# Optimization experiments

Hardware: AMD Instinct MI355X
Metric: run time of the kernel (lower is better)

## Reference

```python
import jax, jax.numpy as jnp
import numpy as np

EMBD = 256
HEAD = 4
HD = EMBD // HEAD  # 64
EPS = 1e-5


def setup_inputs() -> dict:
    key = jax.random.key(0)
    ks = jax.random.split(key, 12)
    s = lambda fan_in: 1.0 / np.sqrt(fan_in)
    return {
        "x": jax.random.normal(ks[0], (16, 1024, EMBD), dtype=jnp.float32),
        # attention params (stored as [in, out])
        "qkv_w": jax.random.uniform(ks[1], (EMBD, 3 * EMBD), jnp.float32, -s(EMBD), s(EMBD)),
        "qkv_b": jax.random.uniform(ks[2], (3 * EMBD,), jnp.float32, -s(EMBD), s(EMBD)),
        "out_w": jax.random.uniform(ks[3], (EMBD, EMBD), jnp.float32, -s(EMBD), s(EMBD)),
        "out_b": jax.random.uniform(ks[4], (EMBD,), jnp.float32, -s(EMBD), s(EMBD)),
        # MLP params
        "fc_w": jax.random.uniform(ks[5], (EMBD, 4 * EMBD), jnp.float32, -s(EMBD), s(EMBD)),
        "fc_b": jax.random.uniform(ks[6], (4 * EMBD,), jnp.float32, -s(EMBD), s(EMBD)),
        "proj_w": jax.random.uniform(ks[7], (4 * EMBD, EMBD), jnp.float32, -s(4 * EMBD), s(4 * EMBD)),
        "proj_b": jax.random.uniform(ks[8], (EMBD,), jnp.float32, -s(4 * EMBD), s(4 * EMBD)),
        # LayerNorm params
        "ln1_g": jnp.ones((EMBD,), jnp.float32),
        "ln1_b": jnp.zeros((EMBD,), jnp.float32),
        "ln2_g": jnp.ones((EMBD,), jnp.float32),
        "ln2_b": jnp.zeros((EMBD,), jnp.float32),
    }


def layer_norm(x, g, b):
    mu = jnp.mean(x, axis=-1, keepdims=True)
    var = jnp.mean(jnp.square(x - mu), axis=-1, keepdims=True)
    return (x - mu) * jax.lax.rsqrt(var + EPS) * g + b


def block_forward(x, qkv_w, qkv_b, out_w, out_b, fc_w, fc_b, proj_w, proj_b,
                  ln1_g, ln1_b, ln2_g, ln2_b):
    B, S, E = x.shape
    # --- attention branch ---
    h = layer_norm(x, ln1_g, ln1_b)
    qkv = h @ qkv_w + qkv_b                       # [B,S,3E]
    q, k, v = jnp.split(qkv, 3, axis=-1)
    q = q.reshape(B, S, HEAD, HD).transpose(0, 2, 1, 3)  # [B,H,S,D]
    k = k.reshape(B, S, HEAD, HD).transpose(0, 2, 1, 3)
    v = v.reshape(B, S, HEAD, HD).transpose(0, 2, 1, 3)
    att = jnp.einsum('bhqd,bhkd->bhqk', q, k) / jnp.sqrt(jnp.float32(HD))
    causal = jnp.tril(jnp.ones((S, S), dtype=bool))
    att = jnp.where(causal, att, -jnp.inf)
    att = jax.nn.softmax(att, axis=-1)
    o = jnp.einsum('bhqk,bhkd->bhqd', att, v)     # [B,H,S,D]
    o = o.transpose(0, 2, 1, 3).reshape(B, S, E)
    x = x + o @ out_w + out_b
    # --- MLP branch (dropout inactive at eval) ---
    h = layer_norm(x, ln2_g, ln2_b)
    h = jax.nn.relu(h @ fc_w + fc_b)
    x = x + h @ proj_w + proj_b
    return x


def reference(x, qkv_w, qkv_b, out_w, out_b, fc_w, fc_b, proj_w, proj_b,
              ln1_g, ln1_b, ln2_g, ln2_b):
    return block_forward(x, qkv_w, qkv_b, out_w, out_b, fc_w, fc_b,
                         proj_w, proj_b, ln1_g, ln1_b, ln2_g, ln2_b)
```

## Files before the change

kernel.cpp:

```cpp
#include <hip/hip_runtime.h>
#include <cstdint>


using f32x4  = __attribute__((ext_vector_type(4))) float;
using f32x16 = __attribute__((ext_vector_type(16))) float;
using s16x8  = __attribute__((ext_vector_type(8))) short;
using s16x4  = __attribute__((ext_vector_type(4))) short;

__device__ inline short f2bf(float f) {
    union { float f; unsigned u; } v{f};
    unsigned r = (v.u + 0x7FFFu + ((v.u >> 16) & 1u)) >> 16;
    return (short)r;
}

__device__ inline int cvt_pk_bf16(float lo, float hi) {
    int d;
    asm("v_cvt_pk_bf16_f32 %0, %1, %2" : "=v"(d) : "v"(lo), "v"(hi));
    return d;
}
__device__ inline void swap32(int& a, int& b) {
    asm("v_permlane32_swap_b32 %0, %1" : "+v"(a), "+v"(b));
}

__device__ inline void gload16(const void* g, void* l) {
    __builtin_amdgcn_global_load_lds(
        (const __attribute__((address_space(1))) void*)g,
        (__attribute__((address_space(3))) void*)l, 16, 0, 0);
}

__global__ __launch_bounds__(256) void prep_kernel(
    const float* __restrict__ qkv_w, const float* __restrict__ out_w,
    const float* __restrict__ fc_w,  const float* __restrict__ proj_w,
    short* __restrict__ wt_qkv, short* __restrict__ wt_out,
    short* __restrict__ wt_fc,  short* __restrict__ wt_proj,
    const float* __restrict__ x, const float* __restrict__ ln1_g,
    const float* __restrict__ ln1_b, short* __restrict__ hout)
{
    __shared__ short T[64][65];
    int id  = blockIdx.x;
    int tid = threadIdx.x;

    if (id < 192) {
        const float* W; short* Wt; int K, N, nt, kt;
        if (id < 48)       { W = qkv_w;  Wt = wt_qkv;  K = 256;  N = 768;  nt = id % 12;        kt = id / 12; }
        else if (id < 64)  { W = out_w;  Wt = wt_out;  K = 256;  N = 256;  nt = (id - 48) & 3;  kt = (id - 48) >> 2; }
        else if (id < 128) { W = fc_w;   Wt = wt_fc;   K = 256;  N = 1024; nt = (id - 64) & 15; kt = (id - 64) >> 4; }
        else               { W = proj_w; Wt = wt_proj; K = 1024; N = 256;  nt = (id - 128) & 3; kt = (id - 128) >> 2; }
        int n0 = nt * 64, k0 = kt * 64;
        int r = tid >> 2, c = (tid & 3) << 4;
        const float* src = W + (size_t)(k0 + r) * N + n0 + c;
#pragma unroll
        for (int u = 0; u < 4; ++u) {
            float4 v = *reinterpret_cast<const float4*>(src + u * 4);
            T[r][c + u * 4 + 0] = f2bf(v.x);
            T[r][c + u * 4 + 1] = f2bf(v.y);
            T[r][c + u * 4 + 2] = f2bf(v.z);
            T[r][c + u * 4 + 3] = f2bf(v.w);
        }
        __syncthreads();
        s16x8 o0, o1;
#pragma unroll
        for (int jj = 0; jj < 8; ++jj) { o0[jj] = T[c + jj][r]; o1[jj] = T[c + 8 + jj][r]; }
        short* dst = Wt + (size_t)(n0 + r) * K + k0 + c;
        *reinterpret_cast<s16x8*>(dst)     = o0;
        *reinterpret_cast<s16x8*>(dst + 8) = o1;
    } else {
        int lane = tid & 63;
        int row  = (id - 192) * 4 + (tid >> 6);
        const float* xr = x + (size_t)row * 256;
        float4 v = *reinterpret_cast<const float4*>(xr + lane * 4);
        float s = v.x + v.y + v.z + v.w;
#pragma unroll
        for (int o2 = 32; o2 >= 1; o2 >>= 1) s += __shfl_xor(s, o2);
        float mu = s * (1.0f / 256.0f);
        float dx = v.x - mu, dy = v.y - mu, dz = v.z - mu, dw = v.w - mu;
        float q = dx * dx + dy * dy + dz * dz + dw * dw;
#pragma unroll
        for (int o2 = 32; o2 >= 1; o2 >>= 1) q += __shfl_xor(q, o2);
        float rstd = rsqrtf(q * (1.0f / 256.0f) + 1e-5f);
        float4 gv = *reinterpret_cast<const float4*>(ln1_g + lane * 4);
        float4 bv = *reinterpret_cast<const float4*>(ln1_b + lane * 4);
        s16x4 ov;
        ov[0] = f2bf(dx * rstd * gv.x + bv.x);
        ov[1] = f2bf(dy * rstd * gv.y + bv.y);
        ov[2] = f2bf(dz * rstd * gv.z + bv.z);
        ov[3] = f2bf(dw * rstd * gv.w + bv.w);
        *reinterpret_cast<s16x4*>(hout + (size_t)row * 256 + lane * 4) = ov;
    }
}

template <int RELU, int RES, int OBF16, int BM, int QKV, int DBUF>
__global__ __launch_bounds__(256) void mgemm_kernel(const short* __restrict__ A,
                                                    const short* __restrict__ Bt,
                                                    const float* __restrict__ bias,
                                                    const float* __restrict__ R,
                                                    void* __restrict__ Cv,
                                                    short* __restrict__ vt,
                                                    int N, int K)
{
    constexpr int MI  = BM / 32;
    constexpr int ASZ = BM * 64;
    constexpr int BSZ = 128 * 64;
    __shared__ short As[(1 + DBUF) * ASZ];
    __shared__ short Bs[(1 + DBUF) * BSZ];

    int tid = threadIdx.x;
    int l   = tid & 63;
    int w   = tid >> 6;
    int lr  = l & 15;
    int lk8 = (l >> 4) << 3;
    int r4  = (l >> 4) << 2;
    int wr  = w >> 1, wc = w & 1;
    int bn  = blockIdx.x * 128, bm = blockIdx.y * BM;

    int scolS = ((l & 7) << 3) ^ ((l >> 3) << 3);
    int srowA = w * (BM / 4) + (l >> 3);
    int srowB = (w << 5) + (l >> 3);
    const short* pa = A  + (size_t)(bm + srowA) * K + scolS;
    const short* pb = Bt + (size_t)(bn + srowB) * K + scolS;
    short* dstA = As + w * (BM / 4) * 64;
    short* dstB = Bs + (w << 11);

    f32x4 acc[MI][4];
#pragma unroll
    for (int mi = 0; mi < MI; ++mi)
#pragma unroll
        for (int ni = 0; ni < 4; ++ni) acc[mi][ni] = (f32x4){0.f, 0.f, 0.f, 0.f};

    int swz = (lr & 7) << 3;
    int cur = 0;

    if (DBUF) {
#pragma unroll
        for (int i = 0; i < BM / 32; ++i)
            gload16(pa + (size_t)(i * 8) * K, dstA + (i << 9));
#pragma unroll
        for (int i = 0; i < 4; ++i)
            gload16(pb + (size_t)(i * 8) * K, dstB + (i << 9));
        __syncthreads();
    }

    for (int k0 = 0; k0 < K; k0 += 64) {
        if (DBUF) {
            if (k0 + 64 < K) {
                int nxt = cur ^ 1;
#pragma unroll
                for (int i = 0; i < BM / 32; ++i)
                    gload16(pa + (size_t)(i * 8) * K + k0 + 64, dstA + nxt * ASZ + (i << 9));
#pragma unroll
                for (int i = 0; i < 4; ++i)
                    gload16(pb + (size_t)(i * 8) * K + k0 + 64, dstB + nxt * BSZ + (i << 9));
            }
        } else {
            __syncthreads();
#pragma unroll
            for (int i = 0; i < BM / 32; ++i)
                gload16(pa + (size_t)(i * 8) * K + k0, dstA + (i << 9));
#pragma unroll
            for (int i = 0; i < 4; ++i)
                gload16(pb + (size_t)(i * 8) * K + k0, dstB + (i << 9));
            __syncthreads();
        }
        const short* curA = As + cur * ASZ;
        const short* curB = Bs + cur * BSZ;
#pragma unroll
        for (int ks = 0; ks < 2; ++ks) {
            s16x8 af[MI], bf[4];
#pragma unroll
            for (int mi = 0; mi < MI; ++mi) {
                int row = wr * (BM / 2) + (mi << 4) + lr;
                af[mi] = *reinterpret_cast<const s16x8*>(
                    &curA[(row << 6) + (((ks << 5) + lk8) ^ swz)]);
            }
#pragma unroll
            for (int ni = 0; ni < 4; ++ni) {
                int row = (wc << 6) + (ni << 4) + lr;
                bf[ni] = *reinterpret_cast<const s16x8*>(
                    &curB[(row << 6) + (((ks << 5) + lk8) ^ swz)]);
            }
            __builtin_amdgcn_s_setprio(1);
#pragma unroll
            for (int mi = 0; mi < MI; ++mi)
#pragma unroll
                for (int ni = 0; ni < 4; ++ni)
                    acc[mi][ni] = __builtin_amdgcn_mfma_f32_16x16x32_bf16(
                        af[mi], bf[ni], acc[mi][ni], 0, 0, 0);
            __builtin_amdgcn_s_setprio(0);
        }
        if (DBUF) {
            __syncthreads();
            cur ^= 1;
        }
    }

    float bv[4];
#pragma unroll
    for (int ni = 0; ni < 4; ++ni)
        bv[ni] = bias[bn + (wc << 6) + (ni << 4) + lr];

#pragma unroll
    for (int mi = 0; mi < MI; ++mi) {
#pragma unroll
        for (int ni = 0; ni < 4; ++ni) {
            int n = bn + (wc << 6) + (ni << 4) + lr;
#pragma unroll
            for (int r = 0; r < 4; ++r) {
                int m = bm + wr * (BM / 2) + (mi << 4) + r4 + r;
                float v = acc[mi][ni][r] + bv[ni];
                if (RELU) v = fmaxf(v, 0.0f);
                if (RES)  v += R[(size_t)m * N + n];
                if (QKV) {
                    if (bn < 512) {
                        ((short*)Cv)[(size_t)m * 512 + n] = f2bf(v);
                    } else {
                        int hh = (n - 512) >> 6, dd = (n - 512) & 63;
                        int bb = m >> 10, ss = m & 1023;
                        vt[(size_t)((((bb << 2) | hh) << 6) | dd) * 1024 + ss] = f2bf(v);
                    }
                } else if (OBF16) {
                    ((short*)Cv)[(size_t)m * N + n] = f2bf(v);
                } else {
                    ((float*)Cv)[(size_t)m * N + n] = v;
                }
            }
        }
    }
}

__global__ __launch_bounds__(256) void oproj_ln_kernel(const short* __restrict__ A,
                                                       const short* __restrict__ Bt,
                                                       const float* __restrict__ bias,
                                                       const float* __restrict__ R,
                                                       float* __restrict__ x1,
                                                       short* __restrict__ h2,
                                                       const float* __restrict__ g,
                                                       const float* __restrict__ bb)
{
    constexpr int ASZ = 64 * 64;
    constexpr int BSZ = 256 * 64;
    __shared__ short As[2 * ASZ];
    __shared__ short Bs[2 * BSZ];

    int tid = threadIdx.x;
    int l   = tid & 63;
    int w   = tid >> 6;
    int lr  = l & 15;
    int lk8 = (l >> 4) << 3;
    int r4  = (l >> 4) << 2;
    int bm  = blockIdx.x * 64;

    int scolS = ((l & 7) << 3) ^ ((l >> 3) << 3);
    const short* pa = A  + (size_t)(bm + (w << 4) + (l >> 3)) * 256 + scolS;
    const short* pb = Bt + (size_t)((w << 6) + (l >> 3)) * 256 + scolS;
    short* dstA = As + (w << 10);
    short* dstB = Bs + (w << 12);

    f32x4 acc[16];
#pragma unroll
    for (int ni = 0; ni < 16; ++ni) acc[ni] = (f32x4){0.f, 0.f, 0.f, 0.f};

    int swz = (lr & 7) << 3;

#pragma unroll
    for (int i = 0; i < 2; ++i)
        gload16(pa + (size_t)(i * 8) * 256, dstA + (i << 9));
#pragma unroll
    for (int i = 0; i < 8; ++i)
        gload16(pb + (size_t)(i * 8) * 256, dstB + (i << 9));
    __syncthreads();

    int cur = 0;
    for (int k0 = 0; k0 < 256; k0 += 64) {
        if (k0 + 64 < 256) {
            int nxt = cur ^ 1;
#pragma unroll
            for (int i = 0; i < 2; ++i)
                gload16(pa + (size_t)(i * 8) * 256 + k0 + 64, dstA + nxt * ASZ + (i << 9));
#pragma unroll
            for (int i = 0; i < 8; ++i)
                gload16(pb + (size_t)(i * 8) * 256 + k0 + 64, dstB + nxt * BSZ + (i << 9));
        }
        const short* curA = As + cur * ASZ;
        const short* curB = Bs + cur * BSZ;
#pragma unroll
        for (int ks = 0; ks < 2; ++ks) {
            int arow = (w << 4) + lr;
            s16x8 af = *reinterpret_cast<const s16x8*>(
                &curA[(arow << 6) + (((ks << 5) + lk8) ^ swz)]);
            __builtin_amdgcn_s_setprio(1);
#pragma unroll
            for (int ni = 0; ni < 16; ++ni) {
                int row = (ni << 4) + lr;
                s16x8 bf = *reinterpret_cast<const s16x8*>(
                    &curB[(row << 6) + (((ks << 5) + lk8) ^ swz)]);
                acc[ni] = __builtin_amdgcn_mfma_f32_16x16x32_bf16(af, bf, acc[ni], 0, 0, 0);
            }
            __builtin_amdgcn_s_setprio(0);
        }
        __syncthreads();
        cur ^= 1;
    }

#pragma unroll
    for (int ni = 0; ni < 16; ++ni) {
        int n = (ni << 4) + lr;
        float bvx = bias[n];
#pragma unroll
        for (int r = 0; r < 4; ++r) {
            int m = bm + (w << 4) + r4 + r;
            acc[ni][r] += bvx + R[(size_t)m * 256 + n];
        }
    }
#pragma unroll
    for (int r = 0; r < 4; ++r) {
        float s = 0.0f;
#pragma unroll
        for (int ni = 0; ni < 16; ++ni) s += acc[ni][r];
        s += __shfl_xor(s, 1); s += __shfl_xor(s, 2);
        s += __shfl_xor(s, 4); s += __shfl_xor(s, 8);
        float mu = s * (1.0f / 256.0f);
        float q = 0.0f;
#pragma unroll
        for (int ni = 0; ni < 16; ++ni) {
            float d = acc[ni][r] - mu;
            q += d * d;
        }
        q += __shfl_xor(q, 1); q += __shfl_xor(q, 2);
        q += __shfl_xor(q, 4); q += __shfl_xor(q, 8);
        float rstd = rsqrtf(q * (1.0f / 256.0f) + 1e-5f);

        int m = bm + (w << 4) + r4 + r;
#pragma unroll
        for (int ni = 0; ni < 16; ++ni) {
            int n = (ni << 4) + lr;
            float v = acc[ni][r];
            x1[(size_t)m * 256 + n] = v;
            h2[(size_t)m * 256 + n] = f2bf((v - mu) * rstd * g[n] + bb[n]);
        }
    }
}

__global__ __launch_bounds__(256, 2) void attn_kernel(const short* __restrict__ qk,
                                                      const short* __restrict__ vt,
                                                      short* __restrict__ o)
{
    constexpr int KSZ = 128 * 64;
    constexpr int VSZ = 64 * 128;
    __shared__ short Ks[2 * KSZ];
    __shared__ short Vs[2 * VSZ];

    int bid  = blockIdx.x;
    int xcd  = bid & 7;
    int j    = bid >> 3;
    int bhg  = j & 7;
    int qidx = j >> 3;
    int qt   = qidx < 4 ? qidx : 11 - qidx;
    int bh   = (bhg << 3) | xcd;
    int b = bh >> 2, h = bh & 3;

    int tid = threadIdx.x;
    int l   = tid & 63;
    int w   = tid >> 6;
    int lq  = l & 31;
    int hg  = l >> 5;

    int krow0 = (w << 3) + (l >> 3);
    int kscol = ((l & 7) << 3) ^ (((l >> 3) & 7) << 3);
    const short* kgp = qk + (size_t)(b * 1024 + krow0) * 512 + 256 + h * 64 + kscol;
    short* dstK = Ks + (w << 3) * 64;
    int vrow0 = (w << 2) + (l >> 4);
    int vscol = ((l & 15) << 3) ^ ((vrow0 & 7) << 3);
    const short* vgp = vt + (size_t)((bh << 6) + vrow0) * 1024 + vscol;
    short* dstV = Vs + (w << 2) * 128;

    const float SC = 0.125f * 1.44269504088896f;

    const short* qrow = qk + (size_t)(b * 1024 + qt * 128 + (w << 5) + lq) * 512
                        + h * 64 + (hg << 3);
    s16x8 qf[4];
#pragma unroll
    for (int ds = 0; ds < 4; ++ds)
        qf[ds] = *reinterpret_cast<const s16x8*>(qrow + 16 * ds);

#pragma unroll
    for (int i = 0; i < 4; ++i) {
        gload16(kgp + (size_t)(i * 32) * 512, dstK + i * 32 * 64);
        gload16(vgp + (size_t)(i * 16) * 1024, dstV + i * 16 * 128);
    }
    __syncthreads();

    float m = -1e30f, lsum = 0.0f;
    f32x16 oacc[2];
#pragma unroll
    for (int dt = 0; dt < 2; ++dt)
#pragma unroll
        for (int r = 0; r < 16; ++r) oacc[dt][r] = 0.0f;
    int qglob = qt * 128 + (w << 5) + lq;
    int cur = 0;
    int niter = qt + 1;

    for (int kt = 0; kt < niter; ++kt) {
        if (kt + 1 < niter) {
            int nxt = cur ^ 1;
#pragma unroll
            for (int i = 0; i < 4; ++i) {
                gload16(kgp + (size_t)((kt + 1) * 128 + i * 32) * 512,
                        dstK + nxt * KSZ + i * 32 * 64);
                gload16(vgp + (size_t)(i * 16) * 1024 + (kt + 1) * 128,
                        dstV + nxt * VSZ + i * 16 * 128);
            }
        }

        f32x16 sv[4];
#pragma unroll
        for (int jt = 0; jt < 4; ++jt)
#pragma unroll
            for (int r = 0; r < 16; ++r) sv[jt][r] = 0.0f;
        __builtin_amdgcn_s_setprio(1);
#pragma unroll
        for (int ds = 0; ds < 4; ++ds) {
#pragma unroll
            for (int jt = 0; jt < 4; ++jt) {
                int row = jt * 32 + lq;
                s16x8 kf = *reinterpret_cast<const s16x8*>(
                    &Ks[cur * KSZ + (row << 6) + ((16 * ds + (hg << 3)) ^ ((row & 7) << 3))]);
                sv[jt] = __builtin_amdgcn_mfma_f32_32x32x16_bf16(kf, qf[ds], sv[jt], 0, 0, 0);
            }
        }
        __builtin_amdgcn_s_setprio(0);
#pragma unroll
        for (int jt = 0; jt < 4; ++jt)
#pragma unroll
            for (int r = 0; r < 16; ++r) sv[jt][r] *= SC;

        if (kt == niter - 1) {
#pragma unroll
            for (int jt = 0; jt < 4; ++jt)
#pragma unroll
                for (int r = 0; r < 16; ++r) {
                    int kg = kt * 128 + jt * 32 + (r & 3) + ((r >> 2) << 3) + (hg << 2);
                    if (kg > qglob) sv[jt][r] = -1e30f;
                }
        }

        float rm = -1e30f;
#pragma unroll
        for (int jt = 0; jt < 4; ++jt)
#pragma unroll
            for (int r = 0; r < 16; ++r) rm = fmaxf(rm, sv[jt][r]);
        rm = fmaxf(rm, __shfl_xor(rm, 32));
        bool big = __any(rm > m + 8.0f);
        float fct = 1.0f;
        if (big) {
            float mn = fmaxf(m, rm);
            fct = exp2f(m - mn);
            m = mn;
        }
        float ps = 0.0f;
#pragma unroll
        for (int jt = 0; jt < 4; ++jt)
#pragma unroll
            for (int r = 0; r < 16; ++r) {
                float p = exp2f(sv[jt][r] - m);
                sv[jt][r] = p;
                ps += p;
            }
        ps += __shfl_xor(ps, 32);
        lsum = lsum * fct + ps;

        if (big) {
#pragma unroll
            for (int r = 0; r < 16; ++r) {
                float f = __shfl(fct, (r & 3) + ((r >> 2) << 3) + (hg << 2));
                oacc[0][r] *= f;
                oacc[1][r] *= f;
            }
        }

#pragma unroll
        for (int jt = 0; jt < 4; ++jt) {
            int x0 = cvt_pk_bf16(sv[jt][0],  sv[jt][1]);
            int x1 = cvt_pk_bf16(sv[jt][2],  sv[jt][3]);
            int y0 = cvt_pk_bf16(sv[jt][4],  sv[jt][5]);
            int y1 = cvt_pk_bf16(sv[jt][6],  sv[jt][7]);
            int z0 = cvt_pk_bf16(sv[jt][8],  sv[jt][9]);
            int z1 = cvt_pk_bf16(sv[jt][10], sv[jt][11]);
            int w0 = cvt_pk_bf16(sv[jt][12], sv[jt][13]);
            int w1 = cvt_pk_bf16(sv[jt][14], sv[jt][15]);
            swap32(x0, y0); swap32(x1, y1);
            swap32(z0, w0); swap32(z1, w1);
            union { int i[4]; s16x8 v; } fA, fB;
            fA.i[0] = x0; fA.i[1] = x1; fA.i[2] = y0; fA.i[3] = y1;
            fB.i[0] = z0; fB.i[1] = z1; fB.i[2] = w0; fB.i[3] = w1;
            __builtin_amdgcn_s_setprio(1);
#pragma unroll
            for (int dt = 0; dt < 2; ++dt) {
                int row = dt * 32 + lq;
                int rs  = (row & 7) << 3;
                s16x8 vfA = *reinterpret_cast<const s16x8*>(
                    &Vs[cur * VSZ + (row << 7) + ((16 * (2 * jt)     + (hg << 3)) ^ rs)]);
                oacc[dt] = __builtin_amdgcn_mfma_f32_32x32x16_bf16(fA.v, vfA, oacc[dt], 0, 0, 0);
                s16x8 vfB = *reinterpret_cast<const s16x8*>(
                    &Vs[cur * VSZ + (row << 7) + ((16 * (2 * jt + 1) + (hg << 3)) ^ rs)]);
                oacc[dt] = __builtin_amdgcn_mfma_f32_32x32x16_bf16(fB.v, vfB, oacc[dt], 0, 0, 0);
            }
            __builtin_amdgcn_s_setprio(0);
        }

        if (kt + 1 < niter) {
            __syncthreads();
            cur ^= 1;
        }
    }

#pragma unroll
    for (int r = 0; r < 16; ++r) {
        int qr  = (r & 3) + ((r >> 2) << 3) + (hg << 2);
        float lv  = __shfl(lsum, qr);
        float inv = 1.0f / lv;
        int q = qt * 128 + (w << 5) + qr;
        short* orow = o + (size_t)(b * 1024 + q) * 256 + h * 64;
        orow[lq]      = f2bf(oacc[0][r] * inv);
        orow[32 + lq] = f2bf(oacc[1][r] * inv);
    }
}

extern "C" void kernel_launch(void* const* d_in, const int* in_sizes, int n_in,
                              void* d_out, int out_size, void* d_ws, size_t ws_size,
                              hipStream_t stream)
{
    const float* x      = (const float*)d_in[0];
    const float* qkv_w  = (const float*)d_in[1];
    const float* qkv_b  = (const float*)d_in[2];
    const float* out_w  = (const float*)d_in[3];
    const float* out_b  = (const float*)d_in[4];
    const float* fc_w   = (const float*)d_in[5];
    const float* fc_b   = (const float*)d_in[6];
    const float* proj_w = (const float*)d_in[7];
    const float* proj_b = (const float*)d_in[8];
    const float* ln1_g  = (const float*)d_in[9];
    const float* ln1_b  = (const float*)d_in[10];
    const float* ln2_g  = (const float*)d_in[11];
    const float* ln2_b  = (const float*)d_in[12];
    float* out = (float*)d_out;

    short* ws = (short*)d_ws;
    short* wt_qkv  = ws;
    short* wt_out  = ws + 196608;
    short* wt_fc   = ws + 262144;
    short* wt_proj = ws + 524288;
    short* bufA    = ws + 786432;
    short* qk_buf  = ws + 4980736;
    short* vt_buf  = ws + 13369344;
    short* h3_buf  = ws + 4980736;

    dim3 blk(256);

    prep_kernel<<<dim3(4288), blk, 0, stream>>>(
        qkv_w, out_w, fc_w, proj_w, wt_qkv, wt_out, wt_fc, wt_proj,
        x, ln1_g, ln1_b, bufA);
    mgemm_kernel<0, 0, 1, 128, 1, 0><<<dim3(6, 128), blk, 0, stream>>>(
        bufA, wt_qkv, qkv_b, nullptr, qk_buf, vt_buf, 768, 256);
    attn_kernel<<<dim3(512), blk, 0, stream>>>(qk_buf, vt_buf, bufA);
    oproj_ln_kernel<<<dim3(256), blk, 0, stream>>>(
        bufA, wt_out, out_b, x, out, bufA, ln2_g, ln2_b);
    mgemm_kernel<1, 0, 1, 128, 0, 0><<<dim3(8, 128), blk, 0, stream>>>(
        bufA, wt_fc, fc_b, nullptr, h3_buf, nullptr, 1024, 256);
    mgemm_kernel<0, 1, 0, 64, 0, 1><<<dim3(2, 256), blk, 0, stream>>>(
        h3_buf, wt_proj, proj_b, out, out, nullptr, 256, 1024);
}
```

Measured before the change: 119.3 us.

## Fuse MLP fc and proj GEMMs into one kernel keeping hidden activations on-chip

Replaces the separate fc+ReLU GEMM and the proj+residual GEMM with a single mlp_kernel. Each block owns 64 rows and loops over eight 128-wide chunks of the hidden dimension. The hidden tile is computed with MFMA, converted to bf16 and redistributed in registers through permlane swaps, then fed straight into the proj MFMAs. This removes the 16Kx1024 bf16 hidden-buffer round trip through global memory and one kernel launch. The cost is only 256 blocks, a large LDS footprint that limits occupancy, and weights re-streamed by every block with no double buffering. The generic GEMM is also specialized to the QKV path.

```diff
diff --git a/kernel.cpp b/kernel.cpp
--- a/kernel.cpp
+++ b/kernel.cpp
@@ -20,6 +20,9 @@
 }
 __device__ inline void swap32(int& a, int& b) {
     asm("v_permlane32_swap_b32 %0, %1" : "+v"(a), "+v"(b));
+}
+__device__ inline void swap16(int& a, int& b) {
+    asm("v_permlane16_swap_b32 %0, %1" : "+v"(a), "+v"(b));
 }
 
 __device__ inline void gload16(const void* g, void* l) {
@@ -89,20 +92,17 @@
     }
 }
 
-template <int RELU, int RES, int OBF16, int BM, int QKV, int DBUF>
-__global__ __launch_bounds__(256) void mgemm_kernel(const short* __restrict__ A,
-                                                    const short* __restrict__ Bt,
-                                                    const float* __restrict__ bias,
-                                                    const float* __restrict__ R,
-                                                    void* __restrict__ Cv,
-                                                    short* __restrict__ vt,
-                                                    int N, int K)
+template <int BM>
+__global__ __launch_bounds__(256) void qkv_gemm_kernel(const short* __restrict__ A,
+                                                       const short* __restrict__ Bt,
+                                                       const float* __restrict__ bias,
+                                                       short* __restrict__ qkout,
+                                                       short* __restrict__ vt,
+                                                       int N, int K)
 {
-    constexpr int MI  = BM / 32;
-    constexpr int ASZ = BM * 64;
-    constexpr int BSZ = 128 * 64;
-    __shared__ short As[(1 + DBUF) * ASZ];
-    __shared__ short Bs[(1 + DBUF) * BSZ];
+    constexpr int MI = BM / 32;
+    __shared__ short As[BM * 64];
+    __shared__ short Bs[128 * 64];
 
     int tid = threadIdx.x;
     int l   = tid & 63;
@@ -128,41 +128,17 @@
         for (int ni = 0; ni < 4; ++ni) acc[mi][ni] = (f32x4){0.f, 0.f, 0.f, 0.f};
 
     int swz = (lr & 7) << 3;
-    int cur = 0;
-
-    if (DBUF) {
+
+    for (int k0 = 0; k0 < K; k0 += 64) {
+        __syncthreads();
 #pragma unroll
         for (int i = 0; i < BM / 32; ++i)
-            gload16(pa + (size_t)(i * 8) * K, dstA + (i << 9));
+            gload16(pa + (size_t)(i * 8) * K + k0, dstA + (i << 9));
 #pragma unroll
         for (int i = 0; i < 4; ++i)
-            gload16(pb + (size_t)(i * 8) * K, dstB + (i << 9));
+            gload16(pb + (size_t)(i * 8) * K + k0, dstB + (i << 9));
         __syncthreads();
-    }
-
-    for (int k0 = 0; k0 < K; k0 += 64) {
-        if (DBUF) {
-            if (k0 + 64 < K) {
-                int nxt = cur ^ 1;
-#pragma unroll
-                for (int i = 0; i < BM / 32; ++i)
-                    gload16(pa + (size_t)(i * 8) * K + k0 + 64, dstA + nxt * ASZ + (i << 9));
-#pragma unroll
-                for (int i = 0; i < 4; ++i)
-                    gload16(pb + (size_t)(i * 8) * K + k0 + 64, dstB + nxt * BSZ + (i << 9));
-            }
-        } else {
-            __syncthreads();
-#pragma unroll
-            for (int i = 0; i < BM / 32; ++i)
-                gload16(pa + (size_t)(i * 8) * K + k0, dstA + (i << 9));
-#pragma unroll
-            for (int i = 0; i < 4; ++i)
-                gload16(pb + (size_t)(i * 8) * K + k0, dstB + (i << 9));
-            __syncthreads();
-        }
-        const short* curA = As + cur * ASZ;
-        const short* curB = Bs + cur * BSZ;
+
 #pragma unroll
         for (int ks = 0; ks < 2; ++ks) {
             s16x8 af[MI], bf[4];
@@ -170,13 +146,13 @@
             for (int mi = 0; mi < MI; ++mi) {
                 int row = wr * (BM / 2) + (mi << 4) + lr;
                 af[mi] = *reinterpret_cast<const s16x8*>(
-                    &curA[(row << 6) + (((ks << 5) + lk8) ^ swz)]);
+                    &As[(row << 6) + (((ks << 5) + lk8) ^ swz)]);
             }
 #pragma unroll
             for (int ni = 0; ni < 4; ++ni) {
                 int row = (wc << 6) + (ni << 4) + lr;
                 bf[ni] = *reinterpret_cast<const s16x8*>(
-                    &curB[(row << 6) + (((ks << 5) + lk8) ^ swz)]);
+                    &Bs[(row << 6) + (((ks << 5) + lk8) ^ swz)]);
             }
             __builtin_amdgcn_s_setprio(1);
 #pragma unroll
@@ -187,10 +163,6 @@
                         af[mi], bf[ni], acc[mi][ni], 0, 0, 0);
             __builtin_amdgcn_s_setprio(0);
         }
-        if (DBUF) {
-            __syncthreads();
-            cur ^= 1;
-        }
     }
 
     float bv[4];
@@ -207,20 +179,12 @@
             for (int r = 0; r < 4; ++r) {
                 int m = bm + wr * (BM / 2) + (mi << 4) + r4 + r;
                 float v = acc[mi][ni][r] + bv[ni];
-                if (RELU) v = fmaxf(v, 0.0f);
-                if (RES)  v += R[(size_t)m * N + n];
-                if (QKV) {
-                    if (bn < 512) {
-                        ((short*)Cv)[(size_t)m * 512 + n] = f2bf(v);
-                    } else {
-                        int hh = (n - 512) >> 6, dd = (n - 512) & 63;
-                        int bb = m >> 10, ss = m & 1023;
-                        vt[(size_t)((((bb << 2) | hh) << 6) | dd) * 1024 + ss] = f2bf(v);
-                    }
-                } else if (OBF16) {
-                    ((short*)Cv)[(size_t)m * N + n] = f2bf(v);
+                if (bn < 512) {
+                    qkout[(size_t)m * 512 + n] = f2bf(v);
                 } else {
-                    ((float*)Cv)[(size_t)m * N + n] = v;
+                    int hh = (n - 512) >> 6, dd = (n - 512) & 63;
+                    int bb = m >> 10, ss = m & 1023;
+                    vt[(size_t)((((bb << 2) | hh) << 6) | dd) * 1024 + ss] = f2bf(v);
                 }
             }
         }
@@ -340,6 +304,137 @@
     }
 }
 
+__global__ __launch_bounds__(256) void mlp_kernel(const short* __restrict__ h2,
+                                                  const short* __restrict__ wfc,
+                                                  const float* __restrict__ fcb,
+                                                  const short* __restrict__ w2,
+                                                  const float* __restrict__ pjb,
+                                                  const float* __restrict__ x1,
+                                                  float* __restrict__ out)
+{
+    __shared__ short H2s[4 * 64 * 64];
+    __shared__ short WFCs[128 * 64];
+    __shared__ short W2s[256 * 128];
+
+    int tid = threadIdx.x;
+    int l   = tid & 63;
+    int w   = tid >> 6;
+    int lr  = l & 15;
+    int lk8 = (l >> 4) << 3;
+    int r4  = (l >> 4) << 2;
+    int bm  = blockIdx.x * 64;
+    int swz = (lr & 7) << 3;
+
+    int scolS = ((l & 7) << 3) ^ ((l >> 3) << 3);
+
+    {
+        const short* pa = h2 + (size_t)(bm + (w << 4) + (l >> 3)) * 256 + scolS;
+#pragma unroll
+        for (int ks4 = 0; ks4 < 4; ++ks4)
+#pragma unroll
+            for (int i = 0; i < 2; ++i)
+                gload16(pa + (size_t)(i * 8) * 256 + ks4 * 64,
+                        H2s + ks4 * 4096 + (w << 10) + (i << 9));
+    }
+
+    int srowB = (w << 5) + (l >> 3);
+    const short* pwfc0 = wfc + (size_t)srowB * 256 + scolS;
+    short* dstWFC = WFCs + (w << 11);
+    int w2colS = ((l & 15) << 3) ^ ((((w << 2) + (l >> 4)) & 7) << 3);
+    const short* pw2 = w2 + (size_t)((w << 2) + (l >> 4)) * 1024 + w2colS;
+    short* dstW2 = W2s + (w << 9);
+
+    f32x4 acc[16];
+#pragma unroll
+    for (int ni = 0; ni < 16; ++ni) acc[ni] = (f32x4){0.f, 0.f, 0.f, 0.f};
+
+    for (int p = 0; p < 8; ++p) {
+        const short* pwfc = pwfc0 + (size_t)(p * 128) * 256;
+
+        f32x4 sv[8];
+#pragma unroll
+        for (int jt = 0; jt < 8; ++jt) sv[jt] = (f32x4){0.f, 0.f, 0.f, 0.f};
+
+        for (int kstep = 0; kstep < 4; ++kstep) {
+            __syncthreads();
+#pragma unroll
+            for (int i = 0; i < 4; ++i)
+                gload16(pwfc + (size_t)(i * 8) * 256 + kstep * 64, dstWFC + (i << 9));
+            __syncthreads();
+
+#pragma unroll
+            for (int ii = 0; ii < 4; ++ii) {
+                int i = kstep * 4 + ii;
+                gload16(pw2 + (size_t)(i * 16) * 1024 + p * 128, dstW2 + (i << 11));
+            }
+
+#pragma unroll
+            for (int ks = 0; ks < 2; ++ks) {
+                int qrow = (w << 4) + lr;
+                s16x8 hf = *reinterpret_cast<const s16x8*>(
+                    &H2s[kstep * 4096 + (qrow << 6) + (((ks << 5) + lk8) ^ swz)]);
+                __builtin_amdgcn_s_setprio(1);
+#pragma unroll
+                for (int jt = 0; jt < 8; ++jt) {
+                    int row = (jt << 4) + lr;
+                    s16x8 wf = *reinterpret_cast<const s16x8*>(
+                        &WFCs[(row << 6) + (((ks << 5) + lk8) ^ swz)]);
+                    sv[jt] = __builtin_amdgcn_mfma_f32_16x16x32_bf16(wf, hf, sv[jt], 0, 0, 0);
+                }
+                __builtin_amdgcn_s_setprio(0);
+            }
+        }
+
+#pragma unroll
+        for (int jt = 0; jt < 8; ++jt) {
+            float4 fb = *reinterpret_cast<const float4*>(fcb + p * 128 + jt * 16 + r4);
+            sv[jt][0] = fmaxf(sv[jt][0] + fb.x, 0.0f);
+            sv[jt][1] = fmaxf(sv[jt][1] + fb.y, 0.0f);
+            sv[jt][2] = fmaxf(sv[jt][2] + fb.z, 0.0f);
+            sv[jt][3] = fmaxf(sv[jt][3] + fb.w, 0.0f);
+        }
+
+        int cpk[8][2];
+#pragma unroll
+        for (int jt = 0; jt < 8; ++jt) {
+            cpk[jt][0] = cvt_pk_bf16(sv[jt][0], sv[jt][1]);
+            cpk[jt][1] = cvt_pk_bf16(sv[jt][2], sv[jt][3]);
+        }
+
+        __syncthreads();
+
+#pragma unroll
+        for (int ks2 = 0; ks2 < 4; ++ks2) {
+            int a0 = cpk[2 * ks2][0],     a1 = cpk[2 * ks2][1];
+            int b0 = cpk[2 * ks2 + 1][0], b1 = cpk[2 * ks2 + 1][1];
+            swap32(a0, b0); swap32(a1, b1);
+            swap16(a0, b0); swap16(a1, b1);
+            union { int i[4]; s16x8 v; } fr;
+            fr.i[0] = a0; fr.i[1] = a1; fr.i[2] = b0; fr.i[3] = b1;
+            __builtin_amdgcn_s_setprio(1);
+#pragma unroll
+            for (int ni = 0; ni < 16; ++ni) {
+                int row = (ni << 4) + lr;
+                s16x8 w2f = *reinterpret_cast<const s16x8*>(
+                    &W2s[(row << 7) + (((ks2 << 5) + lk8) ^ swz)]);
+                acc[ni] = __builtin_amdgcn_mfma_f32_16x16x32_bf16(fr.v, w2f, acc[ni], 0, 0, 0);
+            }
+            __builtin_amdgcn_s_setprio(0);
+        }
+    }
+
+#pragma unroll
+    for (int ni = 0; ni < 16; ++ni) {
+        int n = (ni << 4) + lr;
+        float bvx = pjb[n];
+#pragma unroll
+        for (int r = 0; r < 4; ++r) {
+            int m = bm + (w << 4) + r4 + r;
+            out[(size_t)m * 256 + n] = acc[ni][r] + bvx + x1[(size_t)m * 256 + n];
+        }
+    }
+}
+
 __global__ __launch_bounds__(256, 2) void attn_kernel(const short* __restrict__ qk,
                                                       const short* __restrict__ vt,
                                                       short* __restrict__ o)
@@ -480,18 +575,18 @@
 #pragma unroll
         for (int jt = 0; jt < 4; ++jt) {
             int x0 = cvt_pk_bf16(sv[jt][0],  sv[jt][1]);
-            int x1 = cvt_pk_bf16(sv[jt][2],  sv[jt][3]);
+            int x1v = cvt_pk_bf16(sv[jt][2],  sv[jt][3]);
             int y0 = cvt_pk_bf16(sv[jt][4],  sv[jt][5]);
             int y1 = cvt_pk_bf16(sv[jt][6],  sv[jt][7]);
             int z0 = cvt_pk_bf16(sv[jt][8],  sv[jt][9]);
             int z1 = cvt_pk_bf16(sv[jt][10], sv[jt][11]);
             int w0 = cvt_pk_bf16(sv[jt][12], sv[jt][13]);
             int w1 = cvt_pk_bf16(sv[jt][14], sv[jt][15]);
-            swap32(x0, y0); swap32(x1, y1);
+            swap32(x0, y0); swap32(x1v, y1);
             swap32(z0, w0); swap32(z1, w1);
             union { int i[4]; s16x8 v; } fA, fB;
-            fA.i[0] = x0; fA.i[1] = x1; fA.i[2] = y0; fA.i[3] = y1;
-            fB.i[0] = z0; fB.i[1] = z1; fB.i[2] = w0; fB.i[3] = w1;
+            fA.i[0] = x0; fA.i[1] = x1v; fA.i[2] = y0; fA.i[3] = y1;
+            fB.i[0] = z0; fB.i[1] = z1;  fB.i[2] = w0; fB.i[3] = w1;
             __builtin_amdgcn_s_setprio(1);
 #pragma unroll
             for (int dt = 0; dt < 2; ++dt) {
@@ -552,20 +647,17 @@
     short* bufA    = ws + 786432;
     short* qk_buf  = ws + 4980736;
     short* vt_buf  = ws + 13369344;
-    short* h3_buf  = ws + 4980736;
 
     dim3 blk(256);
 
     prep_kernel<<<dim3(4288), blk, 0, stream>>>(
         qkv_w, out_w, fc_w, proj_w, wt_qkv, wt_out, wt_fc, wt_proj,
         x, ln1_g, ln1_b, bufA);
-    mgemm_kernel<0, 0, 1, 128, 1, 0><<<dim3(6, 128), blk, 0, stream>>>(
-        bufA, wt_qkv, qkv_b, nullptr, qk_buf, vt_buf, 768, 256);
+    qkv_gemm_kernel<128><<<dim3(6, 128), blk, 0, stream>>>(
+        bufA, wt_qkv, qkv_b, qk_buf, vt_buf, 768, 256);
     attn_kernel<<<dim3(512), blk, 0, stream>>>(qk_buf, vt_buf, bufA);
     oproj_ln_kernel<<<dim3(256), blk, 0, stream>>>(
         bufA, wt_out, out_b, x, out, bufA, ln2_g, ln2_b);
-    mgemm_kernel<1, 0, 1, 128, 0, 0><<<dim3(8, 128), blk, 0, stream>>>(
-        bufA, wt_fc, fc_b, nullptr, h3_buf, nullptr, 1024, 256);
-    mgemm_kernel<0, 1, 0, 64, 0, 1><<<dim3(2, 256), blk, 0, stream>>>(
-        h3_buf, wt_proj, proj_b, out, out, nullptr, 256, 1024);
-}
+    mlp_kernel<<<dim3(256), blk, 0, stream>>>(
+        bufA, wt_fc, fc_b, wt_proj, proj_b, out, out);
+}
```

After: 127.8 us. +7.1%, slower.
